# Performance work log

Hardware: AMD Instinct MI355X
Metric: run time of the kernel (lower is better)

## Reference

```python
import jax, jax.numpy as jnp
import numpy as np

D_MODEL = 2048
NUM_HEADS = 16
D_K = D_MODEL // NUM_HEADS

def setup_inputs() -> dict:
    key = jax.random.key(0)
    ks = jax.random.split(key, 5)
    scale = 1.0 / np.sqrt(D_MODEL)
    x = jax.random.normal(ks[0], (4, 2048, D_MODEL), dtype=jnp.float32)
    wq = jax.random.normal(ks[1], (D_MODEL, D_MODEL), dtype=jnp.float32) * scale
    wk = jax.random.normal(ks[2], (D_MODEL, D_MODEL), dtype=jnp.float32) * scale
    wv = jax.random.normal(ks[3], (D_MODEL, D_MODEL), dtype=jnp.float32) * scale
    wo = jax.random.normal(ks[4], (D_MODEL, D_MODEL), dtype=jnp.float32) * scale
    return {"x": x, "wq": wq, "wk": wk, "wv": wv, "wo": wo}

def reference(x, wq, wk, wv, wo):
    # torch Linear (no bias): y = x @ W^T
    B, S, _ = x.shape
    def split_heads(t):
        return t.reshape(B, S, NUM_HEADS, D_K).transpose(0, 2, 1, 3)  # [B,H,S,Dk]
    Q = split_heads(jnp.einsum('bsd,ed->bse', x, wq))
    K = split_heads(jnp.einsum('bsd,ed->bse', x, wk))
    V = split_heads(jnp.einsum('bsd,ed->bse', x, wv))
    scores = jnp.einsum('bhqd,bhkd->bhqk', Q, K) / jnp.sqrt(jnp.float32(D_K))
    attn = jax.nn.softmax(scores, axis=-1)  # dropout=0 (eval semantics)
    out = jnp.einsum('bhqk,bhkd->bhqd', attn, V)
    out = out.transpose(0, 2, 1, 3).reshape(B, S, D_MODEL)
    return jnp.einsum('bsd,ed->bse', out, wo)
```

## Files before the change

kernel.cpp:

```cpp
#include <hip/hip_runtime.h>
#include <math.h>

#define DMODEL 2048
#define NHEADS 16
#define DK     128
#define BATCH  4
#define SEQ    2048
#define MROWS  (BATCH*SEQ)

typedef unsigned short u16;
typedef short s16x8 __attribute__((ext_vector_type(8)));
typedef u16   u16x4 __attribute__((ext_vector_type(4)));
typedef u16   u16x8 __attribute__((ext_vector_type(8)));
typedef float f32x4 __attribute__((ext_vector_type(4)));
typedef unsigned int u32x4 __attribute__((ext_vector_type(4)));

#define MFMA16(a, b, c) __builtin_amdgcn_mfma_f32_16x16x32_bf16((a), (b), (c), 0, 0, 0)

__device__ __forceinline__ u16 f2bf(float f) {
    unsigned u = __builtin_bit_cast(unsigned, f);
    unsigned r = (u + 0x7fffu + ((u >> 16) & 1u)) >> 16;
    return (u16)r;
}
__device__ __forceinline__ u16 f2bf_t(float f) {
    return (u16)(__builtin_bit_cast(unsigned, f) >> 16);
}
__device__ __forceinline__ float bf2f(u16 h) {
    unsigned u = ((unsigned)h) << 16;
    return __builtin_bit_cast(float, u);
}

__device__ __forceinline__ void gld_lds16(const u16* g, u16* l) {
    __builtin_amdgcn_global_load_lds(
        (const __attribute__((address_space(1))) unsigned int*)g,
        (__attribute__((address_space(3))) unsigned int*)l,
        16, 0, 0);
}

__global__ __launch_bounds__(256)
void split_bf16_kernel(const float* __restrict__ src,
                       u16* __restrict__ hi, u16* __restrict__ lo, int n8) {
    const int stride = gridDim.x * blockDim.x;
    for (int i = blockIdx.x * blockDim.x + threadIdx.x; i < n8; i += stride) {
        const float4 f0 = ((const float4*)src)[2 * i];
        const float4 f1 = ((const float4*)src)[2 * i + 1];
        const float f[8] = {f0.x, f0.y, f0.z, f0.w, f1.x, f1.y, f1.z, f1.w};
        u16x8 h8, l8;
#pragma unroll
        for (int j = 0; j < 8; ++j) {
            const u16 hb = f2bf_t(f[j]);
            h8[j] = hb;
            l8[j] = f2bf_t(f[j] - bf2f(hb));
        }
        ((u16x8*)hi)[i] = h8;
        ((u16x8*)lo)[i] = l8;
    }
}

__device__ __forceinline__ void gemm128_split_core(
        const u16* __restrict__ Ahg, const u16* __restrict__ Alg,
        const u16* __restrict__ Bhg, const u16* __restrict__ Blg,
        const int bm, const int bn, f32x4 (&acc)[4][4]) {
    __shared__ __align__(16) u16 Ah[128 * 32];
    __shared__ __align__(16) u16 Al[128 * 32];
    __shared__ __align__(16) u16 Bh[128 * 32];
    __shared__ __align__(16) u16 Bl[128 * 32];

    const int t    = threadIdx.x;
    const int lane = t & 63;
    const int wave = t >> 6;

    const int srow = t >> 2;
    const int skof = (t & 3) * 8;
    const size_t ga0 = (size_t)(bm + srow) * DMODEL + skof;
    const size_t ga1 = (size_t)(bm + srow + 64) * DMODEL + skof;
    const size_t gb0 = (size_t)(bn + srow) * DMODEL + skof;
    const size_t gb1 = (size_t)(bn + srow + 64) * DMODEL + skof;
    const int l0 = srow * 32 + skof;
    const int l1 = l0 + 64 * 32;

    const int lm = lane & 15;
    const int lg = lane >> 4;
    const int wr = (wave >> 1) * 64;
    const int wc = (wave & 1) * 64;
    const int aoff = (wr + lm) * 32 + lg * 8;
    const int boff = (wc + lm) * 32 + lg * 8;

    for (int kt = 0; kt < DMODEL; kt += 32) {
        __syncthreads();
        gld_lds16(Ahg + ga0 + kt, &Ah[l0]);
        gld_lds16(Ahg + ga1 + kt, &Ah[l1]);
        gld_lds16(Alg + ga0 + kt, &Al[l0]);
        gld_lds16(Alg + ga1 + kt, &Al[l1]);
        gld_lds16(Bhg + gb0 + kt, &Bh[l0]);
        gld_lds16(Bhg + gb1 + kt, &Bh[l1]);
        gld_lds16(Blg + gb0 + kt, &Bl[l0]);
        gld_lds16(Blg + gb1 + kt, &Bl[l1]);
        __syncthreads();

        s16x8 af[4], alf[4];
#pragma unroll
        for (int i = 0; i < 4; ++i) {
            af[i]  = *(const s16x8*)&Ah[aoff + i * 16 * 32];
            alf[i] = *(const s16x8*)&Al[aoff + i * 16 * 32];
        }
#pragma unroll
        for (int j = 0; j < 4; ++j) {
            const s16x8 bf  = *(const s16x8*)&Bh[boff + j * 16 * 32];
            const s16x8 blf = *(const s16x8*)&Bl[boff + j * 16 * 32];
#pragma unroll
            for (int i = 0; i < 4; ++i) {
                acc[i][j] = MFMA16(af[i],  bf,  acc[i][j]);
                acc[i][j] = MFMA16(alf[i], bf,  acc[i][j]);
                acc[i][j] = MFMA16(af[i],  blf, acc[i][j]);
            }
        }
    }
}

__global__ __launch_bounds__(256)
void qkv_proj_mfma(const u16* __restrict__ Xhi, const u16* __restrict__ Xlo,
                   const u16* __restrict__ Wh,  const u16* __restrict__ Wl,
                   u16* __restrict__ Qhi, u16* __restrict__ Qlo,
                   u16* __restrict__ Khi, u16* __restrict__ Klo,
                   u16* __restrict__ Vt) {
    const int g  = blockIdx.x >> 4;
    const int nb = blockIdx.x & 15;
    const int bm = blockIdx.y * 128;
    const size_t WE = (size_t)DMODEL * DMODEL;

    f32x4 acc[4][4] = {};
    gemm128_split_core(Xhi, Xlo, Wh + g * WE, Wl + g * WE, bm, nb * 128, acc);

    const int lane = threadIdx.x & 63;
    const int wave = threadIdx.x >> 6;
    const int lm = lane & 15;
    const int lg = lane >> 4;
    const int wr = (wave >> 1) * 64;
    const int wc = (wave & 1) * 64;

    if (g < 2) {
        u16* hiP = (g == 0) ? Qhi : Khi;
        u16* loP = (g == 0) ? Qlo : Klo;
        const float sc = (g == 0) ? 0.08838834764831845f : 1.0f;
#pragma unroll
        for (int i = 0; i < 4; ++i) {
#pragma unroll
            for (int r = 0; r < 4; ++r) {
                const int s  = bm + wr + i * 16 + lg * 4 + r;
                const int bb = s >> 11;
                const size_t base =
                    ((size_t)(bb * NHEADS + nb) * SEQ + (s & 2047)) * DK + wc + lm;
#pragma unroll
                for (int j = 0; j < 4; ++j) {
                    const float y = acc[i][j][r] * sc;
                    const u16 hb = f2bf_t(y);
                    hiP[base + j * 16] = hb;
                    loP[base + j * 16] = f2bf_t(y - bf2f(hb));
                }
            }
        }
    } else {
#pragma unroll
        for (int i = 0; i < 4; ++i) {
            const int s0 = bm + wr + i * 16 + lg * 4;
            const int bb = s0 >> 11;
            const int ss = s0 & 2047;
            const size_t rowb = (size_t)(bb * NHEADS + nb) * DK;
#pragma unroll
            for (int j = 0; j < 4; ++j) {
                u16x4 v;
#pragma unroll
                for (int r = 0; r < 4; ++r) v[r] = f2bf(acc[i][j][r]);
                *(u16x4*)(Vt + (rowb + wc + j * 16 + lm) * SEQ + ss) = v;
            }
        }
    }
}

__global__ __launch_bounds__(256)
void out_proj_mfma(const u16* __restrict__ Ohi, const u16* __restrict__ Olo,
                   const u16* __restrict__ Woh, const u16* __restrict__ Wol,
                   float* __restrict__ out) {
    const int bn = blockIdx.x * 128;
    const int bm = blockIdx.y * 128;
    f32x4 acc[4][4] = {};
    gemm128_split_core(Ohi, Olo, Woh, Wol, bm, bn, acc);

    const int lane = threadIdx.x & 63;
    const int wave = threadIdx.x >> 6;
    const int lm = lane & 15;
    const int lg = lane >> 4;
    const int wr = (wave >> 1) * 64;
    const int wc = (wave & 1) * 64;
#pragma unroll
    for (int i = 0; i < 4; ++i) {
#pragma unroll
        for (int r = 0; r < 4; ++r) {
            const int row = bm + wr + i * 16 + lg * 4 + r;
            float* dst = out + (size_t)row * DMODEL + bn + wc + lm;
#pragma unroll
            for (int j = 0; j < 4; ++j) dst[j * 16] = acc[i][j][r];
        }
    }
}

__global__ __launch_bounds__(256, 4)
void attn_kernel(const u16* __restrict__ Qhi, const u16* __restrict__ Qlo,
                 const u16* __restrict__ KhiG, const u16* __restrict__ KloG,
                 const u16* __restrict__ VtG,
                 u16* __restrict__ Ohi, u16* __restrict__ Olo) {
    __shared__ u16 Khs[32][136];
    __shared__ u16 Kls[32][136];
    __shared__ u16 Vs[128][40];
    __shared__ unsigned int Pb[64][36];

    const int idlin = blockIdx.y * gridDim.x + blockIdx.x;
    const int swz   = (idlin & 7) * 256 + (idlin >> 3);
    const int bh    = swz >> 5;
    const int q0    = (swz & 31) * 64;

    const int t  = threadIdx.x;
    const int l  = t & 63;
    const int w  = t >> 6;
    const int lm = l & 15;
    const int lg = l >> 4;
    const int woff = w * 16;

    s16x8 qh[4], ql[4];
    {
        const size_t qrow = (size_t)bh * SEQ + q0 + woff + lm;
#pragma unroll
        for (int kb = 0; kb < 4; ++kb) {
            const size_t off = qrow * DK + kb * 32 + lg * 8;
            qh[kb] = *(const s16x8*)(Qhi + off);
            ql[kb] = *(const s16x8*)(Qlo + off);
        }
    }

    f32x4 o[8];
#pragma unroll
    for (int nt = 0; nt < 8; ++nt) o[nt] = (f32x4){0.f, 0.f, 0.f, 0.f};
    float m[4] = {-1e30f, -1e30f, -1e30f, -1e30f};
    float lsm[4] = {0.f, 0.f, 0.f, 0.f};

    const int skey = t >> 3;
    const int sdb  = (t & 7) * 16;
    const int vdim = t >> 1;
    const int vkb  = (t & 1) * 16;
    const u16* Kh_base = KhiG + ((size_t)bh * SEQ + skey) * DK + sdb;
    const u16* Kl_base = KloG + ((size_t)bh * SEQ + skey) * DK + sdb;
    const u16* Vt_base = VtG + ((size_t)bh * DK + vdim) * SEQ + vkb;

    u16x8 pk0 = *(const u16x8*)(Kh_base);
    u16x8 pk1 = *(const u16x8*)(Kh_base + 8);
    u16x8 pl0 = *(const u16x8*)(Kl_base);
    u16x8 pl1 = *(const u16x8*)(Kl_base + 8);
    u16x8 pv0 = *(const u16x8*)(Vt_base);
    u16x8 pv1 = *(const u16x8*)(Vt_base + 8);

    for (int kt = 0; kt < SEQ; kt += 32) {
        const int ktn = (kt + 32 < SEQ) ? kt + 32 : 0;
        const u16* khn = Kh_base + (size_t)ktn * DK;
        const u16* kln = Kl_base + (size_t)ktn * DK;
        const u16* vpn = Vt_base + ktn;
        const u16x8 nk0 = *(const u16x8*)khn;
        const u16x8 nk1 = *(const u16x8*)(khn + 8);
        const u16x8 nl0 = *(const u16x8*)kln;
        const u16x8 nl1 = *(const u16x8*)(kln + 8);
        const u16x8 nv0 = *(const u16x8*)vpn;
        const u16x8 nv1 = *(const u16x8*)(vpn + 8);

        __syncthreads();
        *(u16x8*)&Khs[skey][sdb]     = pk0;
        *(u16x8*)&Khs[skey][sdb + 8] = pk1;
        *(u16x8*)&Kls[skey][sdb]     = pl0;
        *(u16x8*)&Kls[skey][sdb + 8] = pl1;
        *(u16x8*)&Vs[vdim][vkb]      = pv0;
        *(u16x8*)&Vs[vdim][vkb + 8]  = pv1;
        __syncthreads();

        f32x4 sacc[2];
#pragma unroll
        for (int nt = 0; nt < 2; ++nt) {
            f32x4 acc = (f32x4){0.f, 0.f, 0.f, 0.f};
#pragma unroll
            for (int kb = 0; kb < 4; ++kb) {
                const s16x8 bh_f = *(const s16x8*)&Khs[nt * 16 + lm][kb * 32 + lg * 8];
                const s16x8 bl_f = *(const s16x8*)&Kls[nt * 16 + lm][kb * 32 + lg * 8];
                acc = MFMA16(qh[kb], bh_f, acc);
                acc = MFMA16(ql[kb], bh_f, acc);
                acc = MFMA16(qh[kb], bl_f, acc);
            }
            sacc[nt] = acc;
        }

        float corr[4], p0[4], p1[4];
#pragma unroll
        for (int r = 0; r < 4; ++r) {
            float v = fmaxf(sacc[0][r], sacc[1][r]);
            v = fmaxf(v, __shfl_xor(v, 1));
            v = fmaxf(v, __shfl_xor(v, 2));
            v = fmaxf(v, __shfl_xor(v, 4));
            v = fmaxf(v, __shfl_xor(v, 8));
            const float mnew = fmaxf(m[r], v);
            corr[r] = __expf(m[r] - mnew);
            m[r] = mnew;
            p0[r] = __expf(sacc[0][r] - mnew);
            p1[r] = __expf(sacc[1][r] - mnew);
            float ls = p0[r] + p1[r];
            ls += __shfl_xor(ls, 1);
            ls += __shfl_xor(ls, 2);
            ls += __shfl_xor(ls, 4);
            ls += __shfl_xor(ls, 8);
            lsm[r] = lsm[r] * corr[r] + ls;
        }
#pragma unroll
        for (int nt = 0; nt < 8; ++nt) {
#pragma unroll
            for (int r = 0; r < 4; ++r) o[nt][r] *= corr[r];
        }

#pragma unroll
        for (int r = 0; r < 4; ++r) {
            const int row = woff + lg * 4 + r;
            const u16 h0 = f2bf_t(p0[r]);
            const u16 l0 = f2bf_t(p0[r] - bf2f(h0));
            Pb[row][lm] = (unsigned)h0 | ((unsigned)l0 << 16);
            const u16 h1 = f2bf_t(p1[r]);
            const u16 l1 = f2bf_t(p1[r] - bf2f(h1));
            Pb[row][16 + lm] = (unsigned)h1 | ((unsigned)l1 << 16);
        }

        const u32x4 r0 = *(const u32x4*)&Pb[woff + lm][lg * 8];
        const u32x4 r1 = *(const u32x4*)&Pb[woff + lm][lg * 8 + 4];
        u32x4 phw, plw;
        phw[0] = (r0[0] & 0xffffu) | (r0[1] << 16);
        phw[1] = (r0[2] & 0xffffu) | (r0[3] << 16);
        phw[2] = (r1[0] & 0xffffu) | (r1[1] << 16);
        phw[3] = (r1[2] & 0xffffu) | (r1[3] << 16);
        plw[0] = (r0[0] >> 16) | (r0[1] & 0xffff0000u);
        plw[1] = (r0[2] >> 16) | (r0[3] & 0xffff0000u);
        plw[2] = (r1[0] >> 16) | (r1[1] & 0xffff0000u);
        plw[3] = (r1[2] >> 16) | (r1[3] & 0xffff0000u);
        const s16x8 pHf = __builtin_bit_cast(s16x8, phw);
        const s16x8 pLf = __builtin_bit_cast(s16x8, plw);

#pragma unroll
        for (int nt = 0; nt < 8; ++nt) {
            const s16x8 vf = *(const s16x8*)&Vs[nt * 16 + lm][lg * 8];
            o[nt] = MFMA16(pHf, vf, o[nt]);
            o[nt] = MFMA16(pLf, vf, o[nt]);
        }

        pk0 = nk0; pk1 = nk1; pl0 = nl0; pl1 = nl1; pv0 = nv0; pv1 = nv1;
    }

    const int bb = bh >> 4;
    const int hh = bh & 15;
    float inv[4];
#pragma unroll
    for (int r = 0; r < 4; ++r) inv[r] = 1.f / lsm[r];
#pragma unroll
    for (int nt = 0; nt < 8; ++nt) {
#pragma unroll
        for (int r = 0; r < 4; ++r) {
            const int qrow = q0 + woff + lg * 4 + r;
            const size_t idx =
                ((size_t)bb * SEQ + qrow) * DMODEL + hh * DK + nt * 16 + lm;
            const float y = o[nt][r] * inv[r];
            const u16 hb = f2bf_t(y);
            Ohi[idx] = hb;
            Olo[idx] = f2bf_t(y - bf2f(hb));
        }
    }
}

extern "C" void kernel_launch(void* const* d_in, const int* in_sizes, int n_in,
                              void* d_out, int out_size, void* d_ws, size_t ws_size,
                              hipStream_t stream) {
    const float* x  = (const float*)d_in[0];
    const float* wq = (const float*)d_in[1];
    const float* wk = (const float*)d_in[2];
    const float* wv = (const float*)d_in[3];
    const float* wo = (const float*)d_in[4];

    const size_t NE = (size_t)MROWS * DMODEL;
    const size_t WE = (size_t)DMODEL * DMODEL;

    u16* Qhi = (u16*)d_ws;
    u16* Qlo = Qhi + NE;
    u16* Khi = Qhi + 2 * NE;
    u16* Klo = Qhi + 3 * NE;
    u16* Vt  = Qhi + 4 * NE;
    u16* Wqkvh = Qhi + 5 * NE;
    u16* Wqkvl = Wqkvh + 3 * WE;
    u16* Ohi = Qhi + 5 * NE;
    u16* Olo = Ohi + NE;
    u16* Woh = Qhi;
    u16* Wol = Woh + WE;
    u16* Xhi = (u16*)d_out;
    u16* Xlo = Xhi + NE;

    dim3 blk(256);
    split_bf16_kernel<<<dim3(1024), blk, 0, stream>>>(x, Xhi, Xlo, (int)(NE / 8));
    split_bf16_kernel<<<dim3(512), blk, 0, stream>>>(wq, Wqkvh, Wqkvl, (int)(WE / 8));
    split_bf16_kernel<<<dim3(512), blk, 0, stream>>>(wk, Wqkvh + WE, Wqkvl + WE, (int)(WE / 8));
    split_bf16_kernel<<<dim3(512), blk, 0, stream>>>(wv, Wqkvh + 2 * WE, Wqkvl + 2 * WE, (int)(WE / 8));

    qkv_proj_mfma<<<dim3(48, 64), blk, 0, stream>>>(Xhi, Xlo, Wqkvh, Wqkvl,
                                                    Qhi, Qlo, Khi, Klo, Vt);
    attn_kernel<<<dim3(SEQ / 64, BATCH * NHEADS), blk, 0, stream>>>(
        Qhi, Qlo, Khi, Klo, Vt, Ohi, Olo);

    split_bf16_kernel<<<dim3(512), blk, 0, stream>>>(wo, Woh, Wol, (int)(WE / 8));
    out_proj_mfma<<<dim3(16, 64), blk, 0, stream>>>(Ohi, Olo, Woh, Wol, (float*)d_out);
}
```

Measured before the change: 1.558 ms.

## Alias K and V shared buffers for higher occupancy and skip rescaling lazily

The attention kernel now shares one LDS buffer between the K hi/lo tiles and the transposed V tile. V is written only after the score MFMAs finish, with extra barriers to order the reuse. This cuts per-block shared memory so launch bounds can ask for 6 blocks per CU instead of 4. Online-softmax rescaling of the accumulators and row sums is now skipped unless some row's new max exceeds the running max by more than 8. The trade-off is two more __syncthreads per key tile and a tighter register budget that may cause spills.

```diff
diff --git a/kernel.cpp b/kernel.cpp
--- a/kernel.cpp
+++ b/kernel.cpp
@@ -205,15 +205,16 @@
     }
 }
 
-__global__ __launch_bounds__(256, 4)
+__global__ __launch_bounds__(256, 6)
 void attn_kernel(const u16* __restrict__ Qhi, const u16* __restrict__ Qlo,
                  const u16* __restrict__ KhiG, const u16* __restrict__ KloG,
                  const u16* __restrict__ VtG,
                  u16* __restrict__ Ohi, u16* __restrict__ Olo) {
-    __shared__ u16 Khs[32][136];
-    __shared__ u16 Kls[32][136];
-    __shared__ u16 Vs[128][40];
+    __shared__ __align__(16) u16 KV[2 * 32 * 136];
     __shared__ unsigned int Pb[64][36];
+#define KHS(r, c) KV[(r) * 136 + (c)]
+#define KLS(r, c) KV[4352 + (r) * 136 + (c)]
+#define VSS(d, k) KV[(d) * 40 + (k)]
 
     const int idlin = blockIdx.y * gridDim.x + blockIdx.x;
     const int swz   = (idlin & 7) * 256 + (idlin >> 3);
@@ -272,12 +273,10 @@
         const u16x8 nv1 = *(const u16x8*)(vpn + 8);
 
         __syncthreads();
-        *(u16x8*)&Khs[skey][sdb]     = pk0;
-        *(u16x8*)&Khs[skey][sdb + 8] = pk1;
-        *(u16x8*)&Kls[skey][sdb]     = pl0;
-        *(u16x8*)&Kls[skey][sdb + 8] = pl1;
-        *(u16x8*)&Vs[vdim][vkb]      = pv0;
-        *(u16x8*)&Vs[vdim][vkb + 8]  = pv1;
+        *(u16x8*)&KHS(skey, sdb)     = pk0;
+        *(u16x8*)&KHS(skey, sdb + 8) = pk1;
+        *(u16x8*)&KLS(skey, sdb)     = pl0;
+        *(u16x8*)&KLS(skey, sdb + 8) = pl1;
         __syncthreads();
 
         f32x4 sacc[2];
@@ -286,8 +285,8 @@
             f32x4 acc = (f32x4){0.f, 0.f, 0.f, 0.f};
 #pragma unroll
             for (int kb = 0; kb < 4; ++kb) {
-                const s16x8 bh_f = *(const s16x8*)&Khs[nt * 16 + lm][kb * 32 + lg * 8];
-                const s16x8 bl_f = *(const s16x8*)&Kls[nt * 16 + lm][kb * 32 + lg * 8];
+                const s16x8 bh_f = *(const s16x8*)&KHS(nt * 16 + lm, kb * 32 + lg * 8);
+                const s16x8 bl_f = *(const s16x8*)&KLS(nt * 16 + lm, kb * 32 + lg * 8);
                 acc = MFMA16(qh[kb], bh_f, acc);
                 acc = MFMA16(ql[kb], bh_f, acc);
                 acc = MFMA16(qh[kb], bl_f, acc);
@@ -295,7 +294,7 @@
             sacc[nt] = acc;
         }
 
-        float corr[4], p0[4], p1[4];
+        float pmax[4];
 #pragma unroll
         for (int r = 0; r < 4; ++r) {
             float v = fmaxf(sacc[0][r], sacc[1][r]);
@@ -303,23 +302,37 @@
             v = fmaxf(v, __shfl_xor(v, 2));
             v = fmaxf(v, __shfl_xor(v, 4));
             v = fmaxf(v, __shfl_xor(v, 8));
-            const float mnew = fmaxf(m[r], v);
-            corr[r] = __expf(m[r] - mnew);
-            m[r] = mnew;
-            p0[r] = __expf(sacc[0][r] - mnew);
-            p1[r] = __expf(sacc[1][r] - mnew);
+            pmax[r] = v;
+        }
+        const bool grow = (pmax[0] - m[0] > 8.f) || (pmax[1] - m[1] > 8.f) ||
+                          (pmax[2] - m[2] > 8.f) || (pmax[3] - m[3] > 8.f);
+        if (__any(grow)) {
+#pragma unroll
+            for (int r = 0; r < 4; ++r) {
+                const float mnew = fmaxf(m[r], pmax[r]);
+                const float corr = __expf(m[r] - mnew);
+                m[r] = mnew;
+                lsm[r] *= corr;
+#pragma unroll
+                for (int nt = 0; nt < 8; ++nt) o[nt][r] *= corr;
+            }
+        }
+        float p0[4], p1[4];
+#pragma unroll
+        for (int r = 0; r < 4; ++r) {
+            p0[r] = __expf(sacc[0][r] - m[r]);
+            p1[r] = __expf(sacc[1][r] - m[r]);
             float ls = p0[r] + p1[r];
             ls += __shfl_xor(ls, 1);
             ls += __shfl_xor(ls, 2);
             ls += __shfl_xor(ls, 4);
             ls += __shfl_xor(ls, 8);
-            lsm[r] = lsm[r] * corr[r] + ls;
-        }
-#pragma unroll
-        for (int nt = 0; nt < 8; ++nt) {
-#pragma unroll
-            for (int r = 0; r < 4; ++r) o[nt][r] *= corr[r];
-        }
+            lsm[r] += ls;
+        }
+
+        __syncthreads();
+        *(u16x8*)&VSS(vdim, vkb)     = pv0;
+        *(u16x8*)&VSS(vdim, vkb + 8) = pv1;
 
 #pragma unroll
         for (int r = 0; r < 4; ++r) {
@@ -346,15 +359,20 @@
         const s16x8 pHf = __builtin_bit_cast(s16x8, phw);
         const s16x8 pLf = __builtin_bit_cast(s16x8, plw);
 
+        __syncthreads();
+
 #pragma unroll
         for (int nt = 0; nt < 8; ++nt) {
-            const s16x8 vf = *(const s16x8*)&Vs[nt * 16 + lm][lg * 8];
+            const s16x8 vf = *(const s16x8*)&VSS(nt * 16 + lm, lg * 8);
             o[nt] = MFMA16(pHf, vf, o[nt]);
             o[nt] = MFMA16(pLf, vf, o[nt]);
         }
 
         pk0 = nk0; pk1 = nk1; pl0 = nl0; pl1 = nl1; pv0 = nv0; pv1 = nv1;
     }
+#undef KHS
+#undef KLS
+#undef VSS
 
     const int bb = bh >> 4;
     const int hh = bh & 15;
```

Result: slower. 3.538 ms (+127.1%).

## Transpose QK^T MFMA layout and add lazy softmax rescaling in attention

Applied to the files above, without the earlier changes.

Swaps the MFMA operand order so each lane holds scores for a single query row. Row max and sum then need only two cross-lane shuffles instead of four per row, with one running max per lane. The output rescale is skipped unless some row's max grows by more than a threshold (8), which removes most of the per-tile multiplies of the O accumulator. The P tile is repacked through a differently shaped LDS buffer to rebuild the PV operand layout. In exchange, exponentials can reach up to e^8 before rescaling, which adds some risk to numeric range and precision.

```diff
diff --git a/kernel.cpp b/kernel.cpp
--- a/kernel.cpp
+++ b/kernel.cpp
@@ -13,6 +13,7 @@
 typedef u16   u16x4 __attribute__((ext_vector_type(4)));
 typedef u16   u16x8 __attribute__((ext_vector_type(8)));
 typedef float f32x4 __attribute__((ext_vector_type(4)));
+typedef unsigned int u32x2 __attribute__((ext_vector_type(2)));
 typedef unsigned int u32x4 __attribute__((ext_vector_type(4)));
 
 #define MFMA16(a, b, c) __builtin_amdgcn_mfma_f32_16x16x32_bf16((a), (b), (c), 0, 0, 0)
@@ -210,10 +211,10 @@
                  const u16* __restrict__ KhiG, const u16* __restrict__ KloG,
                  const u16* __restrict__ VtG,
                  u16* __restrict__ Ohi, u16* __restrict__ Olo) {
-    __shared__ u16 Khs[32][136];
-    __shared__ u16 Kls[32][136];
-    __shared__ u16 Vs[128][40];
-    __shared__ unsigned int Pb[64][36];
+    __shared__ __align__(16) u16 Khs[32][136];
+    __shared__ __align__(16) u16 Kls[32][136];
+    __shared__ __align__(16) u16 Vs[128][40];
+    __shared__ __align__(16) unsigned int Pw[256][12];
 
     const int idlin = blockIdx.y * gridDim.x + blockIdx.x;
     const int swz   = (idlin & 7) * 256 + (idlin >> 3);
@@ -241,8 +242,8 @@
     f32x4 o[8];
 #pragma unroll
     for (int nt = 0; nt < 8; ++nt) o[nt] = (f32x4){0.f, 0.f, 0.f, 0.f};
-    float m[4] = {-1e30f, -1e30f, -1e30f, -1e30f};
-    float lsm[4] = {0.f, 0.f, 0.f, 0.f};
+    float mrun = -1e30f;
+    float lsm  = 0.f;
 
     const int skey = t >> 3;
     const int sdb  = (t & 7) * 16;
@@ -251,6 +252,10 @@
     const u16* Kh_base = KhiG + ((size_t)bh * SEQ + skey) * DK + sdb;
     const u16* Kl_base = KloG + ((size_t)bh * SEQ + skey) * DK + sdb;
     const u16* Vt_base = VtG + ((size_t)bh * DK + vdim) * SEQ + vkb;
+
+    const int prowA = w * 64 + ((2 * lg) & 3) * 16 + lm;
+    const int prowB = w * 64 + ((2 * lg + 1) & 3) * 16 + lm;
+    const int pcol  = (lg < 2) ? 0 : 2;
 
     u16x8 pk0 = *(const u16x8*)(Kh_base);
     u16x8 pk1 = *(const u16x8*)(Kh_base + 8);
@@ -286,63 +291,65 @@
             f32x4 acc = (f32x4){0.f, 0.f, 0.f, 0.f};
 #pragma unroll
             for (int kb = 0; kb < 4; ++kb) {
-                const s16x8 bh_f = *(const s16x8*)&Khs[nt * 16 + lm][kb * 32 + lg * 8];
-                const s16x8 bl_f = *(const s16x8*)&Kls[nt * 16 + lm][kb * 32 + lg * 8];
-                acc = MFMA16(qh[kb], bh_f, acc);
-                acc = MFMA16(ql[kb], bh_f, acc);
-                acc = MFMA16(qh[kb], bl_f, acc);
+                const s16x8 kh_f = *(const s16x8*)&Khs[nt * 16 + lm][kb * 32 + lg * 8];
+                const s16x8 kl_f = *(const s16x8*)&Kls[nt * 16 + lm][kb * 32 + lg * 8];
+                acc = MFMA16(kh_f, qh[kb], acc);
+                acc = MFMA16(kl_f, qh[kb], acc);
+                acc = MFMA16(kh_f, ql[kb], acc);
             }
             sacc[nt] = acc;
         }
 
-        float corr[4], p0[4], p1[4];
+        float pmax = fmaxf(fmaxf(fmaxf(sacc[0][0], sacc[0][1]),
+                                 fmaxf(sacc[0][2], sacc[0][3])),
+                           fmaxf(fmaxf(sacc[1][0], sacc[1][1]),
+                                 fmaxf(sacc[1][2], sacc[1][3])));
+        pmax = fmaxf(pmax, __shfl_xor(pmax, 16));
+        pmax = fmaxf(pmax, __shfl_xor(pmax, 32));
+        if (__any(pmax - mrun > 8.f)) {
+            const float mnew = fmaxf(mrun, pmax);
+            const float corr = __expf(mrun - mnew);
+            mrun = mnew;
+            lsm *= corr;
+            float c4[4];
+#pragma unroll
+            for (int r = 0; r < 4; ++r) c4[r] = __shfl(corr, lg * 4 + r);
+#pragma unroll
+            for (int nt = 0; nt < 8; ++nt) {
+#pragma unroll
+                for (int r = 0; r < 4; ++r) o[nt][r] *= c4[r];
+            }
+        }
+        float p[8];
 #pragma unroll
         for (int r = 0; r < 4; ++r) {
-            float v = fmaxf(sacc[0][r], sacc[1][r]);
-            v = fmaxf(v, __shfl_xor(v, 1));
-            v = fmaxf(v, __shfl_xor(v, 2));
-            v = fmaxf(v, __shfl_xor(v, 4));
-            v = fmaxf(v, __shfl_xor(v, 8));
-            const float mnew = fmaxf(m[r], v);
-            corr[r] = __expf(m[r] - mnew);
-            m[r] = mnew;
-            p0[r] = __expf(sacc[0][r] - mnew);
-            p1[r] = __expf(sacc[1][r] - mnew);
-            float ls = p0[r] + p1[r];
-            ls += __shfl_xor(ls, 1);
-            ls += __shfl_xor(ls, 2);
-            ls += __shfl_xor(ls, 4);
-            ls += __shfl_xor(ls, 8);
-            lsm[r] = lsm[r] * corr[r] + ls;
-        }
-#pragma unroll
-        for (int nt = 0; nt < 8; ++nt) {
-#pragma unroll
-            for (int r = 0; r < 4; ++r) o[nt][r] *= corr[r];
-        }
-
-#pragma unroll
-        for (int r = 0; r < 4; ++r) {
-            const int row = woff + lg * 4 + r;
-            const u16 h0 = f2bf_t(p0[r]);
-            const u16 l0 = f2bf_t(p0[r] - bf2f(h0));
-            Pb[row][lm] = (unsigned)h0 | ((unsigned)l0 << 16);
-            const u16 h1 = f2bf_t(p1[r]);
-            const u16 l1 = f2bf_t(p1[r] - bf2f(h1));
-            Pb[row][16 + lm] = (unsigned)h1 | ((unsigned)l1 << 16);
-        }
-
-        const u32x4 r0 = *(const u32x4*)&Pb[woff + lm][lg * 8];
-        const u32x4 r1 = *(const u32x4*)&Pb[woff + lm][lg * 8 + 4];
-        u32x4 phw, plw;
-        phw[0] = (r0[0] & 0xffffu) | (r0[1] << 16);
-        phw[1] = (r0[2] & 0xffffu) | (r0[3] << 16);
-        phw[2] = (r1[0] & 0xffffu) | (r1[1] << 16);
-        phw[3] = (r1[2] & 0xffffu) | (r1[3] << 16);
-        plw[0] = (r0[0] >> 16) | (r0[1] & 0xffff0000u);
-        plw[1] = (r0[2] >> 16) | (r0[3] & 0xffff0000u);
-        plw[2] = (r1[0] >> 16) | (r1[1] & 0xffff0000u);
-        plw[3] = (r1[2] >> 16) | (r1[3] & 0xffff0000u);
+            p[r]     = __expf(sacc[0][r] - mrun);
+            p[4 + r] = __expf(sacc[1][r] - mrun);
+        }
+        float ls = ((p[0] + p[1]) + (p[2] + p[3])) +
+                   ((p[4] + p[5]) + (p[6] + p[7]));
+        ls += __shfl_xor(ls, 16);
+        ls += __shfl_xor(ls, 32);
+        lsm += ls;
+
+        u32x4 hw, lw;
+#pragma unroll
+        for (int i = 0; i < 4; ++i) {
+            const u16 h0 = f2bf_t(p[2 * i]);
+            const u16 h1 = f2bf_t(p[2 * i + 1]);
+            hw[i] = (unsigned)h0 | ((unsigned)h1 << 16);
+            const u16 e0 = f2bf_t(p[2 * i] - bf2f(h0));
+            const u16 e1 = f2bf_t(p[2 * i + 1] - bf2f(h1));
+            lw[i] = (unsigned)e0 | ((unsigned)e1 << 16);
+        }
+        *(u32x4*)&Pw[t][0] = hw;
+        *(u32x4*)&Pw[t][4] = lw;
+        const u32x2 hA = *(const u32x2*)&Pw[prowA][pcol];
+        const u32x2 hB = *(const u32x2*)&Pw[prowB][pcol];
+        const u32x2 lA = *(const u32x2*)&Pw[prowA][pcol + 4];
+        const u32x2 lB = *(const u32x2*)&Pw[prowB][pcol + 4];
+        const u32x4 phw = {hA[0], hA[1], hB[0], hB[1]};
+        const u32x4 plw = {lA[0], lA[1], lB[0], lB[1]};
         const s16x8 pHf = __builtin_bit_cast(s16x8, phw);
         const s16x8 pLf = __builtin_bit_cast(s16x8, plw);
 
@@ -358,9 +365,10 @@
 
     const int bb = bh >> 4;
     const int hh = bh & 15;
+    const float invl = 1.f / lsm;
     float inv[4];
 #pragma unroll
-    for (int r = 0; r < 4; ++r) inv[r] = 1.f / lsm[r];
+    for (int r = 0; r < 4; ++r) inv[r] = __shfl(invl, lg * 4 + r);
 #pragma unroll
     for (int nt = 0; nt < 8; ++nt) {
 #pragma unroll
```

New measurement: 1.357 ms. 1.15x faster.
